# Kernel optimization log

Hardware: AMD Instinct MI355X
Metric: run time of the kernel (lower is better)

The kernel has to match this reference:

```python
import jax, jax.numpy as jnp
import numpy as np

B, N, IN_DIM = 64, 4096, 128
D = 128          # slot_size
S = 7            # num_slots
ITERS = 3
HID = 256        # mlp_hdim
EPS = 1e-8       # renorm epsilon
LN_EPS = 1e-5    # torch LayerNorm default


def _ln(x, g, b):
    m = jnp.mean(x, axis=-1, keepdims=True)
    v = jnp.mean((x - m) ** 2, axis=-1, keepdims=True)
    return (x - m) * jax.lax.rsqrt(v + LN_EPS) * g + b


def setup_inputs() -> dict:
    key = jax.random.key(0)
    ks = jax.random.split(key, 16)
    s = 0.02
    return {
        "x": jax.random.normal(ks[0], (B, N, IN_DIM), jnp.float32),
        "noise": jax.random.normal(ks[1], (B, S, D), jnp.float32),
        "Wq": jax.random.normal(ks[2], (D, D), jnp.float32) * s,
        "Wk": jax.random.normal(ks[3], (D, IN_DIM), jnp.float32) * s,
        "Wv": jax.random.normal(ks[4], (D, IN_DIM), jnp.float32) * s,
        "ln_in_g": jnp.ones((IN_DIM,), jnp.float32),
        "ln_in_b": jnp.zeros((IN_DIM,), jnp.float32),
        "ln_slots_g": jnp.ones((D,), jnp.float32),
        "ln_slots_b": jnp.zeros((D,), jnp.float32),
        "ln_mlp_g": jnp.ones((D,), jnp.float32),
        "ln_mlp_b": jnp.zeros((D,), jnp.float32),
        "W_ih": jax.random.normal(ks[5], (3 * D, D), jnp.float32) * s,
        "W_hh": jax.random.normal(ks[6], (3 * D, D), jnp.float32) * s,
        "b_ih": jnp.zeros((3 * D,), jnp.float32),
        "b_hh": jnp.zeros((3 * D,), jnp.float32),
        "W1": jax.random.normal(ks[7], (HID, D), jnp.float32) * s,
        "b1": jnp.zeros((HID,), jnp.float32),
        "W2": jax.random.normal(ks[8], (D, HID), jnp.float32) * s,
        "b2": jnp.zeros((D,), jnp.float32),
        "mu": jax.random.normal(ks[9], (1, 1, D), jnp.float32) * s,
        "logsigma": jax.random.normal(ks[10], (1, D), jnp.float32) * s,
    }


def reference(x, noise, Wq, Wk, Wv, ln_in_g, ln_in_b, ln_slots_g, ln_slots_b,
              ln_mlp_g, ln_mlp_b, W_ih, W_hh, b_ih, b_hh, W1, b1, W2, b2,
              mu, logsigma):
    xn = _ln(x, ln_in_g, ln_in_b)              # (B,N,IN)
    k = xn @ Wk.T                              # (B,N,D)
    v = xn @ Wv.T                              # (B,N,D)

    scale = jax.nn.softplus(logsigma)[None] + 1e-5   # (1,1,D)
    slots = mu + scale * noise                 # rsample, (B,S,D)

    def gru(u, h):
        gx = u @ W_ih.T + b_ih                 # (B*S, 3D)
        gh = h @ W_hh.T + b_hh
        xr, xz, xn_ = jnp.split(gx, 3, axis=-1)
        hr, hz, hn = jnp.split(gh, 3, axis=-1)
        r = jax.nn.sigmoid(xr + hr)
        z = jax.nn.sigmoid(xz + hz)
        n = jnp.tanh(xn_ + r * hn)
        return (1.0 - z) * n + z * h

    inv_sqrt_d = D ** -0.5
    for _ in range(ITERS):
        slots_prev = slots
        sn = _ln(slots, ln_slots_g, ln_slots_b)
        q = sn @ Wq.T                          # (B,S,D)
        scores = inv_sqrt_d * jnp.einsum('bnd,bsd->bns', k, q)
        attn = jax.nn.softmax(scores, axis=-1)           # over slots
        attn = attn + EPS
        attn = attn / jnp.sum(attn, axis=1, keepdims=True)  # renorm over inputs
        updates = jnp.einsum('bns,bnd->bsd', attn, v)    # (B,S,D)
        h = gru(updates.reshape(-1, D), slots_prev.reshape(-1, D))
        slots = h.reshape(x.shape[0], S, D)
        slots = _ln(slots, ln_mlp_g, ln_mlp_b)
        slots = slots + (jax.nn.relu(slots @ W1.T + b1) @ W2.T + b2)
    return slots
```

## Files before the change

kernel.cpp:

```cpp
#include <hip/hip_runtime.h>
#include <hip/hip_bf16.h>
#include <stdint.h>

#define B_ 64
#define N_ 4096
#define D_ 128
#define S_ 7
#define EPS_ 1e-8f
#define LN_EPS_ 1e-5f
#define SC_INV 0.08838834764831843f

typedef float  f32x4  __attribute__((ext_vector_type(4)));
typedef __bf16 bf16x8 __attribute__((ext_vector_type(8)));

#define WIH_OFF 0
#define WHH_OFF 49152
#define W1_OFF  98304
#define W2_OFF  131072
#define WQ_OFF  163840
#define WKT_OFF 180224
#define WV_OFF  196608
#define WBF_TOT 212992

__device__ __forceinline__ uint16_t f2bfbits(float f) {
    uint32_t x = __float_as_uint(f);
    return (uint16_t)((x + 0x7fffu + ((x >> 16) & 1u)) >> 16);
}
__device__ __forceinline__ uint32_t pk2(float a, float b) {
    return (uint32_t)f2bfbits(a) | ((uint32_t)f2bfbits(b) << 16);
}

__global__ __launch_bounds__(256) void k_init(
    const float* __restrict__ noise, const float* __restrict__ Wk,
    const float* __restrict__ mu, const float* __restrict__ logsigma,
    const float* __restrict__ Wq, const float* __restrict__ lsg,
    const float* __restrict__ lsb,
    const float* __restrict__ Wih, const float* __restrict__ Whh,
    const float* __restrict__ W1, const float* __restrict__ W2,
    const float* __restrict__ Wv,
    float* __restrict__ slots, uint16_t* __restrict__ kqbf,
    uint16_t* __restrict__ wbf) {
    const int t = threadIdx.x;
    const int tid = blockIdx.x * 256 + t;
    const int row = blockIdx.x;
    const int b = row / 7, s = row - b * 7;
    __shared__ float sn[128], qr[128];
    __shared__ float red[2];
    bool act = t < 128;
    float v = 0.f;
    if (act) {
        float sc = log1pf(__expf(logsigma[t])) + 1e-5f;
        v = mu[t] + sc * noise[row * 128 + t];
        slots[row * 128 + t] = v;
    }
    float sv = act ? v : 0.f;
    #pragma unroll
    for (int m = 1; m < 64; m <<= 1) sv += __shfl_xor(sv, m);
    if (act && (t & 63) == 0) red[t >> 6] = sv;
    __syncthreads();
    float mean = (red[0] + red[1]) * (1.0f / 128.0f);
    __syncthreads();
    float dv = act ? (v - mean) : 0.f;
    float sq = dv * dv;
    #pragma unroll
    for (int m = 1; m < 64; m <<= 1) sq += __shfl_xor(sq, m);
    if (act && (t & 63) == 0) red[t >> 6] = sq;
    __syncthreads();
    float var = (red[0] + red[1]) * (1.0f / 128.0f);
    if (act) sn[t] = dv * rsqrtf(var + LN_EPS_) * lsg[t] + lsb[t];
    __syncthreads();
    if (act) {
        const float4* wr = (const float4*)(Wq + t * 128);
        float acc = 0.f;
        #pragma unroll 8
        for (int j = 0; j < 32; ++j) {
            float4 w = wr[j];
            float4 s4 = *(const float4*)(sn + 4 * j);
            acc += w.x * s4.x + w.y * s4.y + w.z * s4.z + w.w * s4.w;
        }
        qr[t] = acc;
    }
    __syncthreads();
    if (act) {
        float kq = 0.f;
        #pragma unroll 8
        for (int o = 0; o < 128; ++o) kq += qr[o] * Wk[o * 128 + t];
        int elem = (t >> 5) * 512 + (s + 16 * ((t >> 3) & 3)) * 8 + (t & 7);
        kqbf[b * 2048 + elem] = f2bfbits(kq * SC_INV);
    }
    if (tid < 73728) {
        int bb = tid / 1152, rem = tid - bb * 1152;
        int sp = 7 + (rem >> 7), d = rem & 127;
        int elem = (d >> 5) * 512 + (sp + 16 * ((d >> 3) & 3)) * 8 + (d & 7);
        kqbf[bb * 2048 + elem] = 0;
    }
    for (int e = tid; e < WBF_TOT; e += 448 * 256) {
        const float* W; int C, el, mode = 0;
        if (e < WHH_OFF)      { W = Wih; C = 128; el = e; }
        else if (e < W1_OFF)  { W = Whh; C = 128; el = e - WHH_OFF; }
        else if (e < W2_OFF)  { W = W1;  C = 128; el = e - W1_OFF; }
        else if (e < WQ_OFF)  { W = W2;  C = 256; el = e - W2_OFF; }
        else if (e < WKT_OFF) { W = Wq;  C = 128; el = e - WQ_OFF; }
        else if (e < WV_OFF)  { W = Wk;  C = 128; el = e - WKT_OFF; mode = 1; }
        else                  { W = Wv;  C = 128; el = e - WV_OFF; }
        int tile = el >> 9, within = el & 511;
        int lp = within >> 3, j = within & 7;
        int lm_ = lp & 15, qd_ = lp >> 4;
        float w;
        if (!mode) {
            int ktN = C >> 5, ot = tile / ktN, kt = tile - ot * ktN;
            w = W[(ot * 16 + lm_) * C + kt * 32 + qd_ * 8 + j];
        } else {
            int dt = tile >> 2, kt = tile & 3;
            w = W[(kt * 32 + qd_ * 8 + j) * 128 + dt * 16 + lm_];
        }
        wbf[e] = f2bfbits(w);
    }
}

__global__ __launch_bounds__(256) void k_prep_xn(
    const float* __restrict__ x, const float* __restrict__ lng,
    const float* __restrict__ lnb, uint16_t* __restrict__ xn,
    uint16_t* __restrict__ xnB) {
    __shared__ uint16_t sx[64 * 132];
    const int t = threadIdx.x, wv = t >> 6, lane = t & 63;
    const int lm = lane & 15, qd = lane >> 4;
    const long row = (long)blockIdx.x * 64 + wv * 16 + lm;
    const long ntile = (long)blockIdx.x * 4 + wv;
    const float* xp = x + row * 128 + qd * 4;
    f32x4 xa[8];
    #pragma unroll
    for (int c = 0; c < 8; ++c) xa[c] = *(const f32x4*)(xp + c * 16);
    float s = 0.f, sq = 0.f;
    #pragma unroll
    for (int c = 0; c < 8; ++c)
        #pragma unroll
        for (int r = 0; r < 4; ++r) { float v = xa[c][r]; s += v; sq += v * v; }
    s  += __shfl_xor(s, 16);  s  += __shfl_xor(s, 32);
    sq += __shfl_xor(sq, 16); sq += __shfl_xor(sq, 32);
    float mean = s * (1.0f / 128.0f);
    float var  = sq * (1.0f / 128.0f) - mean * mean;
    float rs   = rsqrtf(var + LN_EPS_);
    #pragma unroll
    for (int c = 0; c < 8; ++c) {
        f32x4 g  = *(const f32x4*)(lng + c * 16 + qd * 4);
        f32x4 bb = *(const f32x4*)(lnb + c * 16 + qd * 4);
        float v0 = (xa[c][0] - mean) * rs * g[0] + bb[0];
        float v1 = (xa[c][1] - mean) * rs * g[1] + bb[1];
        float v2 = (xa[c][2] - mean) * rs * g[2] + bb[2];
        float v3 = (xa[c][3] - mean) * rs * g[3] + bb[3];
        uint2 st; st.x = pk2(v0, v1); st.y = pk2(v2, v3);
        long elem = (ntile * 4 + (c >> 1)) * 512
                  + (lm + 16 * (2 * (c & 1) + (qd >> 1))) * 8 + 4 * (qd & 1);
        *(uint2*)(xn + elem) = st;
        *(uint2*)(sx + (wv * 16 + lm) * 132 + c * 16 + qd * 4) = st;
    }
    __syncthreads();
    #pragma unroll
    for (int i = 0; i < 4; ++i) {
        int tix = i * 4 + wv;
        int n32l = tix >> 3, dt = tix & 7;
        uint16_t h[8];
        #pragma unroll
        for (int j = 0; j < 8; ++j)
            h[j] = sx[(n32l * 32 + qd * 8 + j) * 132 + dt * 16 + lm];
        uint4 stv;
        stv.x = (uint32_t)h[0] | ((uint32_t)h[1] << 16);
        stv.y = (uint32_t)h[2] | ((uint32_t)h[3] << 16);
        stv.z = (uint32_t)h[4] | ((uint32_t)h[5] << 16);
        stv.w = (uint32_t)h[6] | ((uint32_t)h[7] << 16);
        *(uint4*)(xnB + ((long)(blockIdx.x * 2 + n32l) * 8 + dt) * 512 + lane * 8) = stv;
    }
}

__global__ __launch_bounds__(256, 4) void k_attn(
    const uint16_t* __restrict__ xn, const uint16_t* __restrict__ xnB,
    const uint16_t* __restrict__ kqbf,
    float* __restrict__ upart, float* __restrict__ cpart) {
    __shared__ __align__(16) uint16_t als[4][16 * 36];
    __shared__ float part[4][7][132];
    __shared__ float bsum[4][8];
    const int t = threadIdx.x, wv = t >> 6, lane = t & 63;
    const int lm = lane & 15, qd = lane >> 4;
    const int b = blockIdx.x >> 4, chunk = blockIdx.x & 15;
    const int ntb = b * 256 + chunk * 16 + wv * 4;
    const int sbase = qd * 4;

    bf16x8 kqf[4];
    #pragma unroll
    for (int k0 = 0; k0 < 4; ++k0)
        kqf[k0] = *(const bf16x8*)(kqbf + b * 2048 + k0 * 512 + lane * 8);

    uint16_t* aw = als[wv];
    f32x4 uacc[8];
    #pragma unroll
    for (int i = 0; i < 8; ++i) uacc[i] = (f32x4){0.f, 0.f, 0.f, 0.f};
    f32x4 csl = {0.f, 0.f, 0.f, 0.f};

    #pragma unroll
    for (int sub = 0; sub < 2; ++sub) {
        f32x4 sc[2];
        #pragma unroll
        for (int nt = 0; nt < 2; ++nt) {
            bf16x8 xf[4];
            #pragma unroll
            for (int k0 = 0; k0 < 4; ++k0)
                xf[k0] = *(const bf16x8*)(xn +
                    ((long)(ntb + sub * 2 + nt) * 4 + k0) * 512 + lane * 8);
            f32x4 acc = {0.f, 0.f, 0.f, 0.f};
            #pragma unroll
            for (int k0 = 0; k0 < 4; ++k0)
                acc = __builtin_amdgcn_mfma_f32_16x16x32_bf16(kqf[k0], xf[k0], acc, 0, 0, 0);
            sc[nt] = acc;
        }
        const long nb = ((long)(ntb >> 1) + sub) * 8;
        bf16x8 bb[8];
        #pragma unroll
        for (int dt = 0; dt < 8; ++dt)
            bb[dt] = *(const bf16x8*)(xnB + (nb + dt) * 512 + lane * 8);
        #pragma unroll
        for (int nt = 0; nt < 2; ++nt) {
            float mx = -1e30f;
            #pragma unroll
            for (int r = 0; r < 4; ++r)
                if (sbase + r < 7) mx = fmaxf(mx, sc[nt][r]);
            mx = fmaxf(mx, __shfl_xor(mx, 16));
            mx = fmaxf(mx, __shfl_xor(mx, 32));
            float e[4], tot = 0.f;
            #pragma unroll
            for (int r = 0; r < 4; ++r) {
                e[r] = (sbase + r < 7) ? __expf(sc[nt][r] - mx) : 0.f;
                tot += e[r];
            }
            tot += __shfl_xor(tot, 16);
            tot += __shfl_xor(tot, 32);
            float inv = 1.0f / tot;
            #pragma unroll
            for (int r = 0; r < 4; ++r) {
                float a_ = (sbase + r < 7) ? e[r] * inv + EPS_ : 0.f;
                csl[r] += a_;
                aw[(sbase + r) * 36 + nt * 16 + lm] = f2bfbits(a_);
            }
        }
        union { uint2 u[2]; bf16x8 v; } cva;
        cva.u[0] = *(const uint2*)(aw + lm * 36 + qd * 8);
        cva.u[1] = *(const uint2*)(aw + lm * 36 + qd * 8 + 4);
        bf16x8 afr = cva.v;
        #pragma unroll
        for (int dt = 0; dt < 8; ++dt)
            uacc[dt] = __builtin_amdgcn_mfma_f32_16x16x32_bf16(afr, bb[dt], uacc[dt], 0, 0, 0);
    }
    #pragma unroll
    for (int m = 1; m < 16; m <<= 1) {
        csl[0] += __shfl_xor(csl[0], m);
        csl[1] += __shfl_xor(csl[1], m);
        csl[2] += __shfl_xor(csl[2], m);
        csl[3] += __shfl_xor(csl[3], m);
    }
    if (lm == 0) {
        #pragma unroll
        for (int r = 0; r < 4; ++r) {
            int s = sbase + r;
            if (s < 7) bsum[wv][s] = csl[r];
        }
    }
    #pragma unroll
    for (int dt = 0; dt < 8; ++dt)
        #pragma unroll
        for (int r = 0; r < 4; ++r) {
            int s = sbase + r;
            if (s < 7) part[wv][s][dt * 16 + lm] = uacc[dt][r];
        }
    __syncthreads();
    if (t < 128) {
        #pragma unroll
        for (int s = 0; s < 7; ++s) {
            float v = part[0][s][t] + part[1][s][t] + part[2][s][t] + part[3][s][t];
            upart[((b * 16 + chunk) * 7 + s) * 128 + t] = v;
        }
    }
    if (t < 7)
        cpart[(b * 16 + chunk) * 7 + t] = bsum[0][t] + bsum[1][t] + bsum[2][t] + bsum[3][t];
}

__global__ __launch_bounds__(256) void k_fused(
    const float* __restrict__ upart, const float* __restrict__ cpart,
    float* __restrict__ slots, const uint16_t* __restrict__ wbf,
    const float* __restrict__ bih, const float* __restrict__ bhh,
    const float* __restrict__ gm, const float* __restrict__ bm,
    const float* __restrict__ b1, const float* __restrict__ b2,
    const float* __restrict__ lsg, const float* __restrict__ lsb,
    uint16_t* __restrict__ kqbf, float* __restrict__ dst, int hasq) {
    __shared__ float uf[16][132];
    __shared__ float hf[16][132];
    __shared__ float slf[16][132];
    __shared__ float hidl[16][264];
    __shared__ float glg[7][776];
    __shared__ float csl[7];
    const int b = blockIdx.x;
    const int t = threadIdx.x, wv = t >> 6, lane = t & 63;
    const int lm = lane & 15, qd = lane >> 4;

    if (t < 7) {
        float c = 0.f;
        #pragma unroll
        for (int i = 0; i < 16; ++i) c += cpart[(b * 16 + i) * 7 + t];
        csl[t] = c;
    }
    for (int idx = t; idx < 896; idx += 256) {
        int s = idx >> 7, d = idx & 127;
        float acc = 0.f;
        #pragma unroll
        for (int i = 0; i < 16; ++i) acc += upart[((b * 16 + i) * 7 + s) * 128 + d];
        slf[s][d] = acc;
        hf[s][d] = slots[(b * 7 + s) * 128 + d];
    }
    __syncthreads();

    {
        bf16x8 apb[4];
        #pragma unroll
        for (int k0 = 0; k0 < 4; ++k0)
            #pragma unroll
            for (int j = 0; j < 8; ++j) apb[k0][j] = (__bf16)slf[lm][k0 * 32 + qd * 8 + j];
        #pragma unroll
        for (int i = 0; i < 2; ++i) {
            int dt = wv * 2 + i;
            f32x4 acc = {0.f, 0.f, 0.f, 0.f};
            #pragma unroll
            for (int k0 = 0; k0 < 4; ++k0) {
                bf16x8 bf = *(const bf16x8*)(wbf + WV_OFF + ((dt * 4 + k0) << 9) + lane * 8);
                acc = __builtin_amdgcn_mfma_f32_16x16x32_bf16(apb[k0], bf, acc, 0, 0, 0);
            }
            #pragma unroll
            for (int r = 0; r < 4; ++r) {
                int s = qd * 4 + r;
                if (s < 7) uf[s][dt * 16 + lm] = acc[r] / csl[s];
            }
        }
    }
    __syncthreads();

    bf16x8 au[4], ah[4];
    #pragma unroll
    for (int k0 = 0; k0 < 4; ++k0)
        #pragma unroll
        for (int j = 0; j < 8; ++j) {
            au[k0][j] = (__bf16)uf[lm][k0 * 32 + qd * 8 + j];
            ah[k0][j] = (__bf16)hf[lm][k0 * 32 + qd * 8 + j];
        }
    {
        const int ih = (wv < 2);
        const uint16_t* W = wbf + (ih ? WIH_OFF : WHH_OFF);
        const int base = ih ? 0 : 384;
        const int w2 = wv & 1;
        #pragma unroll
        for (int i = 0; i < 12; ++i) {
            int ot = w2 * 12 + i;
            f32x4 acc = {0.f, 0.f, 0.f, 0.f};
            #pragma unroll
            for (int k0 = 0; k0 < 4; ++k0) {
                bf16x8 bf = *(const bf16x8*)(W + ((ot * 4 + k0) << 9) + lane * 8);
                acc = __builtin_amdgcn_mfma_f32_16x16x32_bf16(ih ? au[k0] : ah[k0], bf, acc, 0, 0, 0);
            }
            #pragma unroll
            for (int r = 0; r < 4; ++r) {
                int s = qd * 4 + r;
                if (s < 7) glg[s][base + ot * 16 + lm] = acc[r];
            }
        }
    }
    __syncthreads();

    for (int idx = t; idx < 896; idx += 256) {
        int s = idx >> 7, d = idx & 127;
        float xr = glg[s][d] + bih[d];
        float xz = glg[s][128 + d] + bih[128 + d];
        float xg = glg[s][256 + d] + bih[256 + d];
        float hr = glg[s][384 + d] + bhh[d];
        float hz = glg[s][512 + d] + bhh[128 + d];
        float hg = glg[s][640 + d] + bhh[256 + d];
        float r = 1.f / (1.f + __expf(-(xr + hr)));
        float z = 1.f / (1.f + __expf(-(xz + hz)));
        float n = tanhf(xg + r * hg);
        uf[s][d] = (1.f - z) * n + z * hf[s][d];
    }
    __syncthreads();

    for (int s = wv; s < 7; s += 4) {
        float a0 = uf[s][2 * lane], a1 = uf[s][2 * lane + 1];
        float sm = a0 + a1, sq = a0 * a0 + a1 * a1;
        #pragma unroll
        for (int m = 1; m < 64; m <<= 1) { sm += __shfl_xor(sm, m); sq += __shfl_xor(sq, m); }
        float mean = sm * (1.0f / 128.0f);
        float var = sq * (1.0f / 128.0f) - mean * mean;
        float rs = rsqrtf(var + LN_EPS_);
        slf[s][2 * lane]     = (a0 - mean) * rs * gm[2 * lane] + bm[2 * lane];
        slf[s][2 * lane + 1] = (a1 - mean) * rs * gm[2 * lane + 1] + bm[2 * lane + 1];
    }
    __syncthreads();

    bf16x8 as_[4];
    #pragma unroll
    for (int k0 = 0; k0 < 4; ++k0)
        #pragma unroll
        for (int j = 0; j < 8; ++j) as_[k0][j] = (__bf16)slf[lm][k0 * 32 + qd * 8 + j];
    #pragma unroll
    for (int i = 0; i < 4; ++i) {
        int ot = wv * 4 + i;
        f32x4 acc = {0.f, 0.f, 0.f, 0.f};
        #pragma unroll
        for (int k0 = 0; k0 < 4; ++k0) {
            bf16x8 bf = *(const bf16x8*)(wbf + W1_OFF + ((ot * 4 + k0) << 9) + lane * 8);
            acc = __builtin_amdgcn_mfma_f32_16x16x32_bf16(as_[k0], bf, acc, 0, 0, 0);
        }
        #pragma unroll
        for (int r = 0; r < 4; ++r) {
            int s = qd * 4 + r;
            if (s < 7) hidl[s][ot * 16 + lm] = fmaxf(acc[r] + b1[ot * 16 + lm], 0.f);
        }
    }
    __syncthreads();

    bf16x8 ahd[8];
    #pragma unroll
    for (int k0 = 0; k0 < 8; ++k0)
        #pragma unroll
        for (int j = 0; j < 8; ++j) ahd[k0][j] = (__bf16)hidl[lm][k0 * 32 + qd * 8 + j];
    #pragma unroll
    for (int i = 0; i < 2; ++i) {
        int ot = wv * 2 + i;
        f32x4 acc = {0.f, 0.f, 0.f, 0.f};
        #pragma unroll
        for (int k0 = 0; k0 < 8; ++k0) {
            bf16x8 bf = *(const bf16x8*)(wbf + W2_OFF + ((ot * 8 + k0) << 9) + lane * 8);
            acc = __builtin_amdgcn_mfma_f32_16x16x32_bf16(ahd[k0], bf, acc, 0, 0, 0);
        }
        #pragma unroll
        for (int r = 0; r < 4; ++r) {
            int s = qd * 4 + r;
            if (s < 7) {
                float v = slf[s][ot * 16 + lm] + acc[r] + b2[ot * 16 + lm];
                hf[s][ot * 16 + lm] = v;
                dst[(b * 7 + s) * 128 + ot * 16 + lm] = v;
            }
        }
    }
    if (hasq) {
        __syncthreads();
        for (int s = wv; s < 7; s += 4) {
            float a0 = hf[s][2 * lane], a1 = hf[s][2 * lane + 1];
            float sm = a0 + a1, sq = a0 * a0 + a1 * a1;
            #pragma unroll
            for (int m = 1; m < 64; m <<= 1) { sm += __shfl_xor(sm, m); sq += __shfl_xor(sq, m); }
            float mean = sm * (1.0f / 128.0f);
            float var = sq * (1.0f / 128.0f) - mean * mean;
            float rs = rsqrtf(var + LN_EPS_);
            uf[s][2 * lane]     = (a0 - mean) * rs * lsg[2 * lane] + lsb[2 * lane];
            uf[s][2 * lane + 1] = (a1 - mean) * rs * lsg[2 * lane + 1] + lsb[2 * lane + 1];
        }
        __syncthreads();
        bf16x8 an[4];
        #pragma unroll
        for (int k0 = 0; k0 < 4; ++k0)
            #pragma unroll
            for (int j = 0; j < 8; ++j) an[k0][j] = (__bf16)uf[lm][k0 * 32 + qd * 8 + j];
        #pragma unroll
        for (int i = 0; i < 2; ++i) {
            int ot = wv * 2 + i;
            f32x4 acc = {0.f, 0.f, 0.f, 0.f};
            #pragma unroll
            for (int k0 = 0; k0 < 4; ++k0) {
                bf16x8 bf = *(const bf16x8*)(wbf + WQ_OFF + ((ot * 4 + k0) << 9) + lane * 8);
                acc = __builtin_amdgcn_mfma_f32_16x16x32_bf16(an[k0], bf, acc, 0, 0, 0);
            }
            #pragma unroll
            for (int r = 0; r < 4; ++r) {
                int s = qd * 4 + r;
                if (s < 7) slf[s][ot * 16 + lm] = acc[r];
            }
        }
        __syncthreads();
        bf16x8 aq[4];
        #pragma unroll
        for (int k0 = 0; k0 < 4; ++k0)
            #pragma unroll
            for (int j = 0; j < 8; ++j) aq[k0][j] = (__bf16)slf[lm][k0 * 32 + qd * 8 + j];
        #pragma unroll
        for (int i = 0; i < 2; ++i) {
            int dt = wv * 2 + i;
            f32x4 acc = {0.f, 0.f, 0.f, 0.f};
            #pragma unroll
            for (int k0 = 0; k0 < 4; ++k0) {
                bf16x8 bf = *(const bf16x8*)(wbf + WKT_OFF + ((dt * 4 + k0) << 9) + lane * 8);
                acc = __builtin_amdgcn_mfma_f32_16x16x32_bf16(aq[k0], bf, acc, 0, 0, 0);
            }
            #pragma unroll
            for (int r = 0; r < 4; ++r) {
                int s = qd * 4 + r;
                if (s < 7) hidl[s][dt * 16 + lm] = acc[r];
            }
        }
        __syncthreads();
        {
            int kt = t >> 6, lp = t & 63;
            int lmp = lp & 15, qdp = lp >> 4;
            uint16_t h[8];
            #pragma unroll
            for (int j = 0; j < 8; ++j)
                h[j] = (lmp < 7) ? f2bfbits(hidl[lmp][kt * 32 + qdp * 8 + j] * SC_INV) : (uint16_t)0;
            uint4 st;
            st.x = (uint32_t)h[0] | ((uint32_t)h[1] << 16);
            st.y = (uint32_t)h[2] | ((uint32_t)h[3] << 16);
            st.z = (uint32_t)h[4] | ((uint32_t)h[5] << 16);
            st.w = (uint32_t)h[6] | ((uint32_t)h[7] << 16);
            *(uint4*)(kqbf + b * 2048 + t * 8) = st;
        }
    }
}

extern "C" void kernel_launch(void* const* d_in, const int* in_sizes, int n_in,
                              void* d_out, int out_size, void* d_ws, size_t ws_size,
                              hipStream_t stream) {
    const float* x    = (const float*)d_in[0];
    const float* nz   = (const float*)d_in[1];
    const float* Wq   = (const float*)d_in[2];
    const float* Wk   = (const float*)d_in[3];
    const float* Wv   = (const float*)d_in[4];
    const float* ling = (const float*)d_in[5];
    const float* linb = (const float*)d_in[6];
    const float* lsg  = (const float*)d_in[7];
    const float* lsb  = (const float*)d_in[8];
    const float* lmg  = (const float*)d_in[9];
    const float* lmb  = (const float*)d_in[10];
    const float* Wih  = (const float*)d_in[11];
    const float* Whh  = (const float*)d_in[12];
    const float* bih  = (const float*)d_in[13];
    const float* bhh  = (const float*)d_in[14];
    const float* W1   = (const float*)d_in[15];
    const float* b1   = (const float*)d_in[16];
    const float* W2   = (const float*)d_in[17];
    const float* b2   = (const float*)d_in[18];
    const float* mu   = (const float*)d_in[19];
    const float* lsig = (const float*)d_in[20];

    char* wsb = (char*)d_ws;
    uint16_t* xn    = (uint16_t*)(wsb);
    uint16_t* xnB   = (uint16_t*)(wsb + (size_t)67108864);
    uint16_t* wbf   = (uint16_t*)(wsb + (size_t)134217728);
    uint16_t* kqbf  = (uint16_t*)(wsb + (size_t)134643712);
    float*    slots = (float*)  (wsb + (size_t)134905856);
    float*    upart = (float*)  (wsb + (size_t)135135232);
    float*    cpart = (float*)  (wsb + (size_t)138805248);

    k_init<<<448, 256, 0, stream>>>(nz, Wk, mu, lsig, Wq, lsg, lsb,
                                    Wih, Whh, W1, W2, Wv, slots, kqbf, wbf);
    k_prep_xn<<<4096, 256, 0, stream>>>(x, ling, linb, xn, xnB);
    for (int it = 0; it < 3; ++it) {
        float* dst = (it == 2) ? (float*)d_out : slots;
        k_attn<<<1024, 256, 0, stream>>>(xn, xnB, kqbf, upart, cpart);
        k_fused<<<64, 256, 0, stream>>>(upart, cpart, slots, wbf, bih, bhh,
                                        lmg, lmb, b1, b2, lsg, lsb,
                                        kqbf, dst, (it < 2) ? 1 : 0);
    }
}
```

Before: 410.5 us.

## Drop transposed xn copy; build B operand in LDS inside attention kernel

```diff
diff --git a/kernel.cpp b/kernel.cpp
--- a/kernel.cpp
+++ b/kernel.cpp
@@ -30,7 +30,7 @@
     return (uint32_t)f2bfbits(a) | ((uint32_t)f2bfbits(b) << 16);
 }
 
-__global__ __launch_bounds__(256) void k_init(
+__global__ __launch_bounds__(256) void k_init_prep(
     const float* __restrict__ noise, const float* __restrict__ Wk,
     const float* __restrict__ mu, const float* __restrict__ logsigma,
     const float* __restrict__ Wq, const float* __restrict__ lsg,
@@ -39,94 +39,93 @@
     const float* __restrict__ W1, const float* __restrict__ W2,
     const float* __restrict__ Wv,
     float* __restrict__ slots, uint16_t* __restrict__ kqbf,
-    uint16_t* __restrict__ wbf) {
+    uint16_t* __restrict__ wbf,
+    const float* __restrict__ x, const float* __restrict__ lng,
+    const float* __restrict__ lnb, uint16_t* __restrict__ xn) {
     const int t = threadIdx.x;
-    const int tid = blockIdx.x * 256 + t;
-    const int row = blockIdx.x;
-    const int b = row / 7, s = row - b * 7;
-    __shared__ float sn[128], qr[128];
-    __shared__ float red[2];
-    bool act = t < 128;
-    float v = 0.f;
-    if (act) {
-        float sc = log1pf(__expf(logsigma[t])) + 1e-5f;
-        v = mu[t] + sc * noise[row * 128 + t];
-        slots[row * 128 + t] = v;
-    }
-    float sv = act ? v : 0.f;
-    #pragma unroll
-    for (int m = 1; m < 64; m <<= 1) sv += __shfl_xor(sv, m);
-    if (act && (t & 63) == 0) red[t >> 6] = sv;
-    __syncthreads();
-    float mean = (red[0] + red[1]) * (1.0f / 128.0f);
-    __syncthreads();
-    float dv = act ? (v - mean) : 0.f;
-    float sq = dv * dv;
-    #pragma unroll
-    for (int m = 1; m < 64; m <<= 1) sq += __shfl_xor(sq, m);
-    if (act && (t & 63) == 0) red[t >> 6] = sq;
-    __syncthreads();
-    float var = (red[0] + red[1]) * (1.0f / 128.0f);
-    if (act) sn[t] = dv * rsqrtf(var + LN_EPS_) * lsg[t] + lsb[t];
-    __syncthreads();
-    if (act) {
-        const float4* wr = (const float4*)(Wq + t * 128);
-        float acc = 0.f;
-        #pragma unroll 8
-        for (int j = 0; j < 32; ++j) {
-            float4 w = wr[j];
-            float4 s4 = *(const float4*)(sn + 4 * j);
-            acc += w.x * s4.x + w.y * s4.y + w.z * s4.z + w.w * s4.w;
-        }
-        qr[t] = acc;
-    }
-    __syncthreads();
-    if (act) {
-        float kq = 0.f;
-        #pragma unroll 8
-        for (int o = 0; o < 128; ++o) kq += qr[o] * Wk[o * 128 + t];
-        int elem = (t >> 5) * 512 + (s + 16 * ((t >> 3) & 3)) * 8 + (t & 7);
-        kqbf[b * 2048 + elem] = f2bfbits(kq * SC_INV);
-    }
-    if (tid < 73728) {
-        int bb = tid / 1152, rem = tid - bb * 1152;
-        int sp = 7 + (rem >> 7), d = rem & 127;
-        int elem = (d >> 5) * 512 + (sp + 16 * ((d >> 3) & 3)) * 8 + (d & 7);
-        kqbf[bb * 2048 + elem] = 0;
-    }
-    for (int e = tid; e < WBF_TOT; e += 448 * 256) {
-        const float* W; int C, el, mode = 0;
-        if (e < WHH_OFF)      { W = Wih; C = 128; el = e; }
-        else if (e < W1_OFF)  { W = Whh; C = 128; el = e - WHH_OFF; }
-        else if (e < W2_OFF)  { W = W1;  C = 128; el = e - W1_OFF; }
-        else if (e < WQ_OFF)  { W = W2;  C = 256; el = e - W2_OFF; }
-        else if (e < WKT_OFF) { W = Wq;  C = 128; el = e - WQ_OFF; }
-        else if (e < WV_OFF)  { W = Wk;  C = 128; el = e - WKT_OFF; mode = 1; }
-        else                  { W = Wv;  C = 128; el = e - WV_OFF; }
-        int tile = el >> 9, within = el & 511;
-        int lp = within >> 3, j = within & 7;
-        int lm_ = lp & 15, qd_ = lp >> 4;
-        float w;
-        if (!mode) {
-            int ktN = C >> 5, ot = tile / ktN, kt = tile - ot * ktN;
-            w = W[(ot * 16 + lm_) * C + kt * 32 + qd_ * 8 + j];
-        } else {
-            int dt = tile >> 2, kt = tile & 3;
-            w = W[(kt * 32 + qd_ * 8 + j) * 128 + dt * 16 + lm_];
-        }
-        wbf[e] = f2bfbits(w);
-    }
-}
-
-__global__ __launch_bounds__(256) void k_prep_xn(
-    const float* __restrict__ x, const float* __restrict__ lng,
-    const float* __restrict__ lnb, uint16_t* __restrict__ xn,
-    uint16_t* __restrict__ xnB) {
-    __shared__ uint16_t sx[64 * 132];
-    const int t = threadIdx.x, wv = t >> 6, lane = t & 63;
+    if (blockIdx.x < 448) {
+        __shared__ float sn[128], qr[128];
+        __shared__ float red[2];
+        const int tid = blockIdx.x * 256 + t;
+        const int row = blockIdx.x;
+        const int b = row / 7, s = row - b * 7;
+        bool act = t < 128;
+        float v = 0.f;
+        if (act) {
+            float sc = log1pf(__expf(logsigma[t])) + 1e-5f;
+            v = mu[t] + sc * noise[row * 128 + t];
+            slots[row * 128 + t] = v;
+        }
+        float sv = act ? v : 0.f;
+        #pragma unroll
+        for (int m = 1; m < 64; m <<= 1) sv += __shfl_xor(sv, m);
+        if (act && (t & 63) == 0) red[t >> 6] = sv;
+        __syncthreads();
+        float mean = (red[0] + red[1]) * (1.0f / 128.0f);
+        __syncthreads();
+        float dv = act ? (v - mean) : 0.f;
+        float sq = dv * dv;
+        #pragma unroll
+        for (int m = 1; m < 64; m <<= 1) sq += __shfl_xor(sq, m);
+        if (act && (t & 63) == 0) red[t >> 6] = sq;
+        __syncthreads();
+        float var = (red[0] + red[1]) * (1.0f / 128.0f);
+        if (act) sn[t] = dv * rsqrtf(var + LN_EPS_) * lsg[t] + lsb[t];
+        __syncthreads();
+        if (act) {
+            const float4* wr = (const float4*)(Wq + t * 128);
+            float acc = 0.f;
+            #pragma unroll 8
+            for (int j = 0; j < 32; ++j) {
+                float4 w = wr[j];
+                float4 s4 = *(const float4*)(sn + 4 * j);
+                acc += w.x * s4.x + w.y * s4.y + w.z * s4.z + w.w * s4.w;
+            }
+            qr[t] = acc;
+        }
+        __syncthreads();
+        if (act) {
+            float kq = 0.f;
+            #pragma unroll 8
+            for (int o = 0; o < 128; ++o) kq += qr[o] * Wk[o * 128 + t];
+            int elem = (t >> 5) * 512 + (s + 16 * ((t >> 3) & 3)) * 8 + (t & 7);
+            kqbf[b * 2048 + elem] = f2bfbits(kq * SC_INV);
+        }
+        if (tid < 73728) {
+            int bb = tid / 1152, rem = tid - bb * 1152;
+            int sp = 7 + (rem >> 7), d = rem & 127;
+            int elem = (d >> 5) * 512 + (sp + 16 * ((d >> 3) & 3)) * 8 + (d & 7);
+            kqbf[bb * 2048 + elem] = 0;
+        }
+        for (int e = tid; e < WBF_TOT; e += 448 * 256) {
+            const float* W; int C, el, mode = 0;
+            if (e < WHH_OFF)      { W = Wih; C = 128; el = e; }
+            else if (e < W1_OFF)  { W = Whh; C = 128; el = e - WHH_OFF; }
+            else if (e < W2_OFF)  { W = W1;  C = 128; el = e - W1_OFF; }
+            else if (e < WQ_OFF)  { W = W2;  C = 256; el = e - W2_OFF; }
+            else if (e < WKT_OFF) { W = Wq;  C = 128; el = e - WQ_OFF; }
+            else if (e < WV_OFF)  { W = Wk;  C = 128; el = e - WKT_OFF; mode = 1; }
+            else                  { W = Wv;  C = 128; el = e - WV_OFF; }
+            int tile = el >> 9, within = el & 511;
+            int lp = within >> 3, j = within & 7;
+            int lm_ = lp & 15, qd_ = lp >> 4;
+            float w;
+            if (!mode) {
+                int ktN = C >> 5, ot = tile / ktN, kt = tile - ot * ktN;
+                w = W[(ot * 16 + lm_) * C + kt * 32 + qd_ * 8 + j];
+            } else {
+                int dt = tile >> 2, kt = tile & 3;
+                w = W[(kt * 32 + qd_ * 8 + j) * 128 + dt * 16 + lm_];
+            }
+            wbf[e] = f2bfbits(w);
+        }
+        return;
+    }
+    const int pid = blockIdx.x - 448;
+    const int wv = t >> 6, lane = t & 63;
     const int lm = lane & 15, qd = lane >> 4;
-    const long row = (long)blockIdx.x * 64 + wv * 16 + lm;
-    const long ntile = (long)blockIdx.x * 4 + wv;
+    const long row = (long)pid * 64 + wv * 16 + lm;
+    const long ntile = (long)pid * 4 + wv;
     const float* xp = x + row * 128 + qd * 4;
     f32x4 xa[8];
     #pragma unroll
@@ -153,32 +152,14 @@
         long elem = (ntile * 4 + (c >> 1)) * 512
                   + (lm + 16 * (2 * (c & 1) + (qd >> 1))) * 8 + 4 * (qd & 1);
         *(uint2*)(xn + elem) = st;
-        *(uint2*)(sx + (wv * 16 + lm) * 132 + c * 16 + qd * 4) = st;
-    }
-    __syncthreads();
-    #pragma unroll
-    for (int i = 0; i < 4; ++i) {
-        int tix = i * 4 + wv;
-        int n32l = tix >> 3, dt = tix & 7;
-        uint16_t h[8];
-        #pragma unroll
-        for (int j = 0; j < 8; ++j)
-            h[j] = sx[(n32l * 32 + qd * 8 + j) * 132 + dt * 16 + lm];
-        uint4 stv;
-        stv.x = (uint32_t)h[0] | ((uint32_t)h[1] << 16);
-        stv.y = (uint32_t)h[2] | ((uint32_t)h[3] << 16);
-        stv.z = (uint32_t)h[4] | ((uint32_t)h[5] << 16);
-        stv.w = (uint32_t)h[6] | ((uint32_t)h[7] << 16);
-        *(uint4*)(xnB + ((long)(blockIdx.x * 2 + n32l) * 8 + dt) * 512 + lane * 8) = stv;
     }
 }
 
 __global__ __launch_bounds__(256, 4) void k_attn(
-    const uint16_t* __restrict__ xn, const uint16_t* __restrict__ xnB,
-    const uint16_t* __restrict__ kqbf,
+    const uint16_t* __restrict__ xn, const uint16_t* __restrict__ kqbf,
     float* __restrict__ upart, float* __restrict__ cpart) {
+    __shared__ __align__(16) uint16_t stage[4][32 * 132];
     __shared__ __align__(16) uint16_t als[4][16 * 36];
-    __shared__ float part[4][7][132];
     __shared__ float bsum[4][8];
     const int t = threadIdx.x, wv = t >> 6, lane = t & 63;
     const int lm = lane & 15, qd = lane >> 4;
@@ -191,6 +172,8 @@
     for (int k0 = 0; k0 < 4; ++k0)
         kqf[k0] = *(const bf16x8*)(kqbf + b * 2048 + k0 * 512 + lane * 8);
 
+    uint16_t* xw = stage[wv];
+    float* prt = (float*)stage[wv];
     uint16_t* aw = als[wv];
     f32x4 uacc[8];
     #pragma unroll
@@ -199,25 +182,31 @@
 
     #pragma unroll
     for (int sub = 0; sub < 2; ++sub) {
+        bf16x8 xf[2][4];
+        #pragma unroll
+        for (int nt = 0; nt < 2; ++nt)
+            #pragma unroll
+            for (int k0 = 0; k0 < 4; ++k0)
+                xf[nt][k0] = *(const bf16x8*)(xn +
+                    ((long)(ntb + sub * 2 + nt) * 4 + k0) * 512 + lane * 8);
+        #pragma unroll
+        for (int nt = 0; nt < 2; ++nt)
+            #pragma unroll
+            for (int k0 = 0; k0 < 4; ++k0) {
+                int base = (nt * 16 + lm) * 132 + k0 * 32 + qd * 8;
+                const uint2* src = (const uint2*)&xf[nt][k0];
+                *(uint2*)(xw + base)     = src[0];
+                *(uint2*)(xw + base + 4) = src[1];
+            }
         f32x4 sc[2];
         #pragma unroll
         for (int nt = 0; nt < 2; ++nt) {
-            bf16x8 xf[4];
+            f32x4 acc = {0.f, 0.f, 0.f, 0.f};
             #pragma unroll
             for (int k0 = 0; k0 < 4; ++k0)
-                xf[k0] = *(const bf16x8*)(xn +
-                    ((long)(ntb + sub * 2 + nt) * 4 + k0) * 512 + lane * 8);
-            f32x4 acc = {0.f, 0.f, 0.f, 0.f};
-            #pragma unroll
-            for (int k0 = 0; k0 < 4; ++k0)
-                acc = __builtin_amdgcn_mfma_f32_16x16x32_bf16(kqf[k0], xf[k0], acc, 0, 0, 0);
+                acc = __builtin_amdgcn_mfma_f32_16x16x32_bf16(kqf[k0], xf[nt][k0], acc, 0, 0, 0);
             sc[nt] = acc;
         }
-        const long nb = ((long)(ntb >> 1) + sub) * 8;
-        bf16x8 bb[8];
-        #pragma unroll
-        for (int dt = 0; dt < 8; ++dt)
-            bb[dt] = *(const bf16x8*)(xnB + (nb + dt) * 512 + lane * 8);
         #pragma unroll
         for (int nt = 0; nt < 2; ++nt) {
             float mx = -1e30f;
@@ -247,8 +236,13 @@
         cva.u[1] = *(const uint2*)(aw + lm * 36 + qd * 8 + 4);
         bf16x8 afr = cva.v;
         #pragma unroll
-        for (int dt = 0; dt < 8; ++dt)
-            uacc[dt] = __builtin_amdgcn_mfma_f32_16x16x32_bf16(afr, bb[dt], uacc[dt], 0, 0, 0);
+        for (int dt = 0; dt < 8; ++dt) {
+            bf16x8 bfr;
+            #pragma unroll
+            for (int j = 0; j < 8; ++j)
+                bfr[j] = ((const __bf16*)xw)[(qd * 8 + j) * 132 + dt * 16 + lm];
+            uacc[dt] = __builtin_amdgcn_mfma_f32_16x16x32_bf16(afr, bfr, uacc[dt], 0, 0, 0);
+        }
     }
     #pragma unroll
     for (int m = 1; m < 16; m <<= 1) {
@@ -269,14 +263,18 @@
         #pragma unroll
         for (int r = 0; r < 4; ++r) {
             int s = sbase + r;
-            if (s < 7) part[wv][s][dt * 16 + lm] = uacc[dt][r];
+            if (s < 7) prt[s * 132 + dt * 16 + lm] = uacc[dt][r];
         }
     __syncthreads();
     if (t < 128) {
+        const float* p0 = (const float*)stage[0];
+        const float* p1 = (const float*)stage[1];
+        const float* p2 = (const float*)stage[2];
+        const float* p3 = (const float*)stage[3];
         #pragma unroll
         for (int s = 0; s < 7; ++s) {
-            float v = part[0][s][t] + part[1][s][t] + part[2][s][t] + part[3][s][t];
-            upart[((b * 16 + chunk) * 7 + s) * 128 + t] = v;
+            int o = s * 132 + t;
+            upart[((b * 16 + chunk) * 7 + s) * 128 + t] = p0[o] + p1[o] + p2[o] + p3[o];
         }
     }
     if (t < 7)
@@ -546,19 +544,18 @@
 
     char* wsb = (char*)d_ws;
     uint16_t* xn    = (uint16_t*)(wsb);
-    uint16_t* xnB   = (uint16_t*)(wsb + (size_t)67108864);
-    uint16_t* wbf   = (uint16_t*)(wsb + (size_t)134217728);
-    uint16_t* kqbf  = (uint16_t*)(wsb + (size_t)134643712);
-    float*    slots = (float*)  (wsb + (size_t)134905856);
-    float*    upart = (float*)  (wsb + (size_t)135135232);
-    float*    cpart = (float*)  (wsb + (size_t)138805248);
-
-    k_init<<<448, 256, 0, stream>>>(nz, Wk, mu, lsig, Wq, lsg, lsb,
-                                    Wih, Whh, W1, W2, Wv, slots, kqbf, wbf);
-    k_prep_xn<<<4096, 256, 0, stream>>>(x, ling, linb, xn, xnB);
+    uint16_t* wbf   = (uint16_t*)(wsb + (size_t)67108864);
+    uint16_t* kqbf  = (uint16_t*)(wsb + (size_t)67534848);
+    float*    slots = (float*)  (wsb + (size_t)67796992);
+    float*    upart = (float*)  (wsb + (size_t)68026368);
+    float*    cpart = (float*)  (wsb + (size_t)71696384);
+
+    k_init_prep<<<4544, 256, 0, stream>>>(nz, Wk, mu, lsig, Wq, lsg, lsb,
+                                          Wih, Whh, W1, W2, Wv, slots, kqbf, wbf,
+                                          x, ling, linb, xn);
     for (int it = 0; it < 3; ++it) {
         float* dst = (it == 2) ? (float*)d_out : slots;
-        k_attn<<<1024, 256, 0, stream>>>(xn, xnB, kqbf, upart, cpart);
+        k_attn<<<1024, 256, 0, stream>>>(xn, kqbf, upart, cpart);
         k_fused<<<64, 256, 0, stream>>>(upart, cpart, slots, wbf, bih, bhh,
                                         lmg, lmb, b1, b2, lsg, lsb,
                                         kqbf, dst, (it < 2) ? 1 : 0);
```

Result: faster. 352.8 us (-14.1%).
